# Kernel tuning notes

Measured on AMD Instinct MI355X. Metric: run time of the kernel, lower is better.

The kernel has to match this reference:

```python
import jax, jax.numpy as jnp
import numpy as np

N = 200_000   # nodes
E = 6_400_000 # edges (avg degree 32)
G = 1024      # graphs in the batch
H = 8         # hidden dim


def setup_inputs() -> dict:
    key = jax.random.key(0)
    ks = jax.random.split(key, 13)
    x = jax.random.normal(ks[0], (N, 1), dtype=jnp.float32)
    edge_index = jax.random.randint(ks[1], (2, E), 0, N, dtype=jnp.int32)
    batch = jnp.sort(jax.random.randint(ks[2], (N,), 0, G, dtype=jnp.int32))
    s = 0.3
    params = dict(
        W1a=s * jax.random.normal(ks[3], (1, H), jnp.float32),
        b1a=jnp.zeros((H,), jnp.float32),
        W1b=s * jax.random.normal(ks[4], (H, H), jnp.float32),
        b1b=jnp.zeros((H,), jnp.float32),
        W2a=s * jax.random.normal(ks[5], (H, H), jnp.float32),
        b2a=jnp.zeros((H,), jnp.float32),
        W2b=s * jax.random.normal(ks[6], (H, H), jnp.float32),
        b2b=jnp.zeros((H,), jnp.float32),
        Wfc=s * jax.random.normal(ks[7], (H, 1), jnp.float32),
        bfc=jnp.zeros((1,), jnp.float32),
    )
    return dict(x=x, edge_index=edge_index, batch=batch, **params)


def _gin_layer(h, src, dst, Wa, ba, Wb, bb):
    # GINConv with eps=0: mlp(x_i + sum_{j->i} x_j); messages aggregated at dst=edge_index[1]
    agg = jax.ops.segment_sum(h[src], dst, num_segments=N)  # [N, d]
    z = h + agg
    z = jax.nn.relu(z @ Wa + ba)
    return z @ Wb + bb


def reference(x, edge_index, batch, W1a, b1a, W1b, b1b, W2a, b2a, W2b, b2b, Wfc, bfc):
    src, dst = edge_index[0], edge_index[1]
    h = _gin_layer(x, src, dst, W1a, b1a, W1b, b1b)   # [N, 8]
    h = jax.nn.elu(h)
    h = _gin_layer(h, src, dst, W2a, b2a, W2b, b2b)   # [N, 8]
    # global mean pool over graphs
    sums = jax.ops.segment_sum(h, batch, num_segments=G)                  # [G, 8]
    counts = jax.ops.segment_sum(jnp.ones((N,), h.dtype), batch, num_segments=G)
    pooled = sums / jnp.maximum(counts, 1.0)[:, None]
    out = jax.nn.sigmoid(pooled @ Wfc + bfc)          # [G, 1]
    return out.reshape(-1)
```

## Files before the change

### kernel.cpp

```cpp
#include <hip/hip_runtime.h>
#include <hip/hip_fp8.h>
#include <math.h>

#define H 8
#define NBLKA 256
#define BTH 1024
#define BSH 8
#define BCAP 9216
#define TS 1024
#define SCAP 25600
#define POOLG 128

__device__ __forceinline__ unsigned f2fp8(float f) {
    __hip_fp8_e4m3 q(f);
    return (unsigned)q.__x;
}
__device__ __forceinline__ float fp8f(unsigned v) {
    __hip_fp8_e4m3 q;
    q.__x = (__hip_fp8_storage_t)v;
    return (float)q;
}
#if defined(__has_builtin)
#if __has_builtin(__builtin_amdgcn_cvt_pk_f32_fp8)
#define HAVE_CVT_PK_FP8 1
#endif
#endif
typedef float v2f __attribute__((ext_vector_type(2)));
__device__ __forceinline__ void unpack8(float* f, uint2 v) {
#ifdef HAVE_CVT_PK_FP8
    v2f f01 = __builtin_amdgcn_cvt_pk_f32_fp8((int)v.x, false);
    v2f f23 = __builtin_amdgcn_cvt_pk_f32_fp8((int)v.x, true);
    v2f f45 = __builtin_amdgcn_cvt_pk_f32_fp8((int)v.y, false);
    v2f f67 = __builtin_amdgcn_cvt_pk_f32_fp8((int)v.y, true);
    f[0] = f01.x; f[1] = f01.y; f[2] = f23.x; f[3] = f23.y;
    f[4] = f45.x; f[5] = f45.y; f[6] = f67.x; f[7] = f67.y;
#else
    f[0] = fp8f(v.x & 255u);         f[1] = fp8f((v.x >> 8) & 255u);
    f[2] = fp8f((v.x >> 16) & 255u); f[3] = fp8f(v.x >> 24);
    f[4] = fp8f(v.y & 255u);         f[5] = fp8f((v.y >> 8) & 255u);
    f[6] = fp8f((v.y >> 16) & 255u); f[7] = fp8f(v.y >> 24);
#endif
}
__device__ __forceinline__ void acc8(float* a, uint2 v) {
    float f[8];
    unpack8(f, v);
#pragma unroll
    for (int j = 0; j < 8; j++) a[j] += f[j];
}

__global__ __launch_bounds__(BTH) void scatterK(const int* __restrict__ ei, int E, int NB,
                                                int chunk, int* __restrict__ cursor,
                                                unsigned* __restrict__ packed) {
    __shared__ unsigned ss[SCAP];
    __shared__ int cnt[1024], sc[1024], base[1024], cur[1024];
    int t = threadIdx.x, blk = blockIdx.x;
    cnt[t] = 0;
    __syncthreads();
    int s = blk * chunk, e = min(E, s + chunk);
    for (int i = s + t; i < e; i += BTH)
        atomicAdd(&cnt[__builtin_nontemporal_load(ei + E + i) >> BSH], 1);
    __syncthreads();
    int c = cnt[t];
    sc[t] = c;
    __syncthreads();
    for (int off = 1; off < 1024; off <<= 1) {
        int v = (t >= off) ? sc[t - off] : 0;
        __syncthreads();
        sc[t] += v;
        __syncthreads();
    }
    cur[t] = sc[t] - c;
    base[t] = (t < NB && c > 0) ? atomicAdd(&cursor[t], c) : 0;
    __syncthreads();
    for (int i = s + t; i < e; i += BTH) {
        int src = __builtin_nontemporal_load(ei + i);
        int dst = __builtin_nontemporal_load(ei + E + i);
        int pos = atomicAdd(&cur[dst >> BSH], 1);
        ss[pos] = ((unsigned)src << 8) | (unsigned)(dst & 255);
    }
    __syncthreads();
    int wave = t >> 6, lane = t & 63;
    for (int j = wave; j < NB; j += (BTH >> 6)) {
        int n = cnt[j];
        int ls = sc[j] - n;
        int bs = base[j];
        int m = min(n, BCAP - bs);
        int gs = j * BCAP + bs;
        for (int k = lane; k < m; k += 64)
            packed[gs + k] = ss[ls + k];
    }
}

__global__ void sortL1K(unsigned* __restrict__ packed, const int* __restrict__ bucketCnt,
                        const float* __restrict__ x, int N,
                        const float* __restrict__ W1a, const float* __restrict__ b1a,
                        const float* __restrict__ W1b, const float* __restrict__ b1b,
                        int* __restrict__ nodeStart, uint2* __restrict__ h1) {
    __shared__ unsigned ss[BCAP];
    __shared__ float sv[BCAP];
    __shared__ int cnt[256], sb[256], cur[256];
    __shared__ float sW1a[H], sb1a[H], sW1b[H * H], sb1b[H];
    int t = threadIdx.x, b = blockIdx.x;
    if (t < 256) cnt[t] = 0;
    else if (t < 256 + H) { int j = t - 256; sW1a[j] = W1a[j]; sb1a[j] = b1a[j]; sb1b[j] = b1b[j]; }
    else if (t < 256 + H + H * H) { int j = t - 256 - H; sW1b[j] = W1b[j]; }
    __syncthreads();
    int s = b * BCAP;
    int n_e = min(bucketCnt[b], BCAP);
    unsigned pk[9];
    float xr[9];
#pragma unroll
    for (int k = 0; k < 9; k++) {
        int i = t + (k << 10);
        if (i < n_e) {
            unsigned p = packed[s + i];
            pk[k] = p;
            xr[k] = x[p >> 8];
            atomicAdd(&cnt[p & 255u], 1);
        }
    }
    __syncthreads();
    if (t < 256) sb[t] = cnt[t];
    __syncthreads();
    for (int off = 1; off < 256; off <<= 1) {
        int add = (t < 256 && t >= off) ? sb[t - off] : 0;
        __syncthreads();
        if (t < 256) sb[t] += add;
        __syncthreads();
    }
    if (t < 256) {
        int excl = sb[t] - cnt[t];
        cur[t] = excl;
        nodeStart[(b << BSH) + t] = s + excl;
    }
    __syncthreads();
#pragma unroll
    for (int k = 0; k < 9; k++) {
        int i = t + (k << 10);
        if (i < n_e) {
            unsigned p = pk[k];
            int pos = atomicAdd(&cur[p & 255u], 1);
            ss[pos] = p >> 8;
            sv[pos] = xr[k];
        }
    }
    __syncthreads();
    for (int i = t; i < n_e; i += TS) packed[s + i] = ss[i];
    int node = t >> 2, q4 = t & 3;
    int gn = (b << BSH) + node;
    float xself = x[min(gn, N - 1)];
    int lo = sb[node] - cnt[node], hi = sb[node];
    float sum = 0.f;
    for (int k = lo + q4; k < hi; k += 4) sum += sv[k];
    sum += __shfl_xor(sum, 1, 64);
    sum += __shfl_xor(sum, 2, 64);
    if (q4 == 0 && gn < N) {
        float z = xself + sum;
        float tv[H];
#pragma unroll
        for (int k = 0; k < H; k++) tv[k] = fmaxf(fmaf(z, sW1a[k], sb1a[k]), 0.f);
        float hv[H];
#pragma unroll
        for (int j = 0; j < H; j++) {
            float a = sb1b[j];
#pragma unroll
            for (int k = 0; k < H; k++) a += tv[k] * sW1b[k * H + j];
            hv[j] = a > 0.f ? a : (expf(a) - 1.f);
        }
        uint2 o;
        o.x = f2fp8(hv[0]) | (f2fp8(hv[1]) << 8) | (f2fp8(hv[2]) << 16) | (f2fp8(hv[3]) << 24);
        o.y = f2fp8(hv[4]) | (f2fp8(hv[5]) << 8) | (f2fp8(hv[6]) << 16) | (f2fp8(hv[7]) << 24);
        h1[gn] = o;
    }
}

__global__ __launch_bounds__(1024, 8) void layer2K(
        const unsigned* __restrict__ packed, const int* __restrict__ nodeStart,
        const int* __restrict__ bucketCnt, const uint2* __restrict__ h1, int N,
        const float* __restrict__ W2a, const float* __restrict__ b2a,
        const float* __restrict__ W2b, const float* __restrict__ b2b,
        const int* __restrict__ batch, float* __restrict__ sumsCnt) {
    __shared__ unsigned ss[BCAP];
    __shared__ int sNS[257];
    __shared__ float pool[POOLG * 9];
    __shared__ float sW2a[H * H], sb2a[H], sW2b[H * H], sb2b[H];
    int t = threadIdx.x, b = blockIdx.x;
    int s = b * BCAP;
    int n_e = min(bucketCnt[b], BCAP);
    for (int i = t; i < n_e; i += 1024)
        ss[i] = __builtin_nontemporal_load(packed + s + i);
    if (t < 256) sNS[t] = nodeStart[(b << BSH) + t] - s;
    if (t == 256) sNS[256] = 0;
    if (t < H) { sb2a[t] = b2a[t]; sb2b[t] = b2b[t]; }
    else if (t >= 64 && t < 64 + H * H) sW2a[t - 64] = W2a[t - 64];
    else if (t >= 192 && t < 192 + H * H) sW2b[t - 192] = W2b[t - 192];
    __syncthreads();
    if (t == 0) sNS[256] = n_e;
    __syncthreads();
    int node = t >> 2, q4 = t & 3;
    int gn = (b << BSH) + node;
    uint2 vself = h1[gn];
    int lo = sNS[node], hi = sNS[node + 1];
    float a[H] = {0.f, 0.f, 0.f, 0.f, 0.f, 0.f, 0.f, 0.f};
    for (int k0 = lo + q4; k0 < hi; k0 += 32) {
        unsigned i0 = ss[k0];
        unsigned i1 = ss[min(k0 + 4,  hi - 1)];
        unsigned i2 = ss[min(k0 + 8,  hi - 1)];
        unsigned i3 = ss[min(k0 + 12, hi - 1)];
        unsigned i4 = ss[min(k0 + 16, hi - 1)];
        unsigned i5 = ss[min(k0 + 20, hi - 1)];
        unsigned i6 = ss[min(k0 + 24, hi - 1)];
        unsigned i7 = ss[min(k0 + 28, hi - 1)];
        uint2 v0 = h1[i0];
        uint2 v1 = h1[i1];
        uint2 v2 = h1[i2];
        uint2 v3 = h1[i3];
        uint2 v4 = h1[i4];
        uint2 v5 = h1[i5];
        uint2 v6 = h1[i6];
        uint2 v7 = h1[i7];
        acc8(a, v0);
        if (k0 + 4  < hi) acc8(a, v1);
        if (k0 + 8  < hi) acc8(a, v2);
        if (k0 + 12 < hi) acc8(a, v3);
        if (k0 + 16 < hi) acc8(a, v4);
        if (k0 + 20 < hi) acc8(a, v5);
        if (k0 + 24 < hi) acc8(a, v6);
        if (k0 + 28 < hi) acc8(a, v7);
    }
#pragma unroll
    for (int j = 0; j < H; j++) {
        a[j] += __shfl_xor(a[j], 1, 64);
        a[j] += __shfl_xor(a[j], 2, 64);
    }
    bool valid = (q4 == 0) && (gn < N);
    float h2[H];
    int g = 0;
    if (valid) {
        float zs[H];
        unpack8(zs, vself);
        float z[H];
#pragma unroll
        for (int j = 0; j < H; j++) z[j] = zs[j] + a[j];
        float tv[H];
#pragma unroll
        for (int k = 0; k < H; k++) {
            float acc = sb2a[k];
#pragma unroll
            for (int j = 0; j < H; j++) acc += z[j] * sW2a[j * H + k];
            tv[k] = fmaxf(acc, 0.f);
        }
#pragma unroll
        for (int j = 0; j < H; j++) {
            float acc = sb2b[j];
#pragma unroll
            for (int k = 0; k < H; k++) acc += tv[k] * sW2b[k * H + j];
            h2[j] = acc;
        }
        g = batch[gn];
    }
    int gfirst = batch[min(b << BSH, N - 1)];
    int glast  = batch[min((b << BSH) + 255, N - 1)];
    int span = glast - gfirst + 1;
    if (span <= POOLG) {
        int span9 = span * 9;
        for (int j = t; j < span9; j += 1024) pool[j] = 0.f;
        __syncthreads();
        if (valid) {
            float* p = &pool[(g - gfirst) * 9];
#pragma unroll
            for (int j = 0; j < H; j++) atomicAdd(p + j, h2[j]);
            atomicAdd(p + 8, 1.f);
        }
        __syncthreads();
        for (int j = t; j < span9; j += 1024)
            atomicAdd(&sumsCnt[(size_t)gfirst * 9 + j], pool[j]);
    } else if (valid) {
        float* p = &sumsCnt[(size_t)g * 9];
#pragma unroll
        for (int j = 0; j < H; j++) atomicAdd(p + j, h2[j]);
        atomicAdd(p + 8, 1.f);
    }
}

__global__ void finalK(const float* __restrict__ sumsCnt, const float* __restrict__ Wfc,
                       const float* __restrict__ bfc, float* __restrict__ out, int G) {
    int g = blockIdx.x * blockDim.x + threadIdx.x;
    if (g >= G) return;
    const float* s = &sumsCnt[(size_t)g * 9];
    float c = fmaxf(s[8], 1.f);
    float dot = 0.f;
#pragma unroll
    for (int j = 0; j < H; j++) dot += s[j] * Wfc[j];
    float a = dot / c + bfc[0];
    out[g] = 1.f / (1.f + expf(-a));
}

__global__ void edge_agg1(const int* __restrict__ ei, const float* __restrict__ x,
                          float* __restrict__ agg1, int E) {
    int e = blockIdx.x * blockDim.x + threadIdx.x;
    if (e >= E) return;
    atomicAdd(&agg1[ei[E + e]], x[ei[e]]);
}
__global__ void node1F(const float* __restrict__ x, const float* __restrict__ agg1,
                       const float* __restrict__ W1a, const float* __restrict__ b1a,
                       const float* __restrict__ W1b, const float* __restrict__ b1b,
                       float* __restrict__ h1, int N) {
    int n = blockIdx.x * blockDim.x + threadIdx.x;
    if (n >= N) return;
    float z = x[n] + agg1[n];
    float tv[H];
#pragma unroll
    for (int k = 0; k < H; k++) tv[k] = fmaxf(z * W1a[k] + b1a[k], 0.f);
#pragma unroll
    for (int j = 0; j < H; j++) {
        float acc = b1b[j];
#pragma unroll
        for (int k = 0; k < H; k++) acc += tv[k] * W1b[k * H + j];
        h1[(size_t)n * H + j] = acc > 0.f ? acc : (expf(acc) - 1.f);
    }
}
__global__ void edge_agg2(const int* __restrict__ ei, const float* __restrict__ h1,
                          float* __restrict__ agg2, int E) {
    long long i = (long long)blockIdx.x * blockDim.x + threadIdx.x;
    if (i >= (long long)E * H) return;
    int e = (int)(i >> 3), k = (int)(i & 7);
    atomicAdd(&agg2[(size_t)ei[E + e] * H + k], h1[(size_t)ei[e] * H + k]);
}
__global__ void node2F(const float* __restrict__ h1, const float* __restrict__ agg2,
                       const float* __restrict__ W2a, const float* __restrict__ b2a,
                       const float* __restrict__ W2b, const float* __restrict__ b2b,
                       const int* __restrict__ batch,
                       float* __restrict__ sums, float* __restrict__ counts, int N) {
    int n = blockIdx.x * blockDim.x + threadIdx.x;
    if (n >= N) return;
    float z[H], tv[H];
#pragma unroll
    for (int j = 0; j < H; j++) z[j] = h1[(size_t)n * H + j] + agg2[(size_t)n * H + j];
#pragma unroll
    for (int k = 0; k < H; k++) {
        float a = b2a[k];
#pragma unroll
        for (int j = 0; j < H; j++) a += z[j] * W2a[j * H + k];
        tv[k] = fmaxf(a, 0.f);
    }
    int g = batch[n];
#pragma unroll
    for (int j = 0; j < H; j++) {
        float a = b2b[j];
#pragma unroll
        for (int k = 0; k < H; k++) a += tv[k] * W2b[k * H + j];
        atomicAdd(&sums[(size_t)g * H + j], a);
    }
    atomicAdd(&counts[g], 1.f);
}
__global__ void finalF(const float* __restrict__ sums, const float* __restrict__ counts,
                       const float* __restrict__ Wfc, const float* __restrict__ bfc,
                       float* __restrict__ out, int G) {
    int g = blockIdx.x * blockDim.x + threadIdx.x;
    if (g >= G) return;
    float c = fmaxf(counts[g], 1.f);
    float acc = bfc[0];
#pragma unroll
    for (int j = 0; j < H; j++) acc += (sums[(size_t)g * H + j] / c) * Wfc[j];
    out[g] = 1.f / (1.f + expf(-acc));
}

extern "C" void kernel_launch(void* const* d_in, const int* in_sizes, int n_in,
                              void* d_out, int out_size, void* d_ws, size_t ws_size,
                              hipStream_t stream) {
    const float* x    = (const float*)d_in[0];
    const int*   ei   = (const int*)d_in[1];
    const int*   batch= (const int*)d_in[2];
    const float* W1a  = (const float*)d_in[3];
    const float* b1a  = (const float*)d_in[4];
    const float* W1b  = (const float*)d_in[5];
    const float* b1b  = (const float*)d_in[6];
    const float* W2a  = (const float*)d_in[7];
    const float* b2a  = (const float*)d_in[8];
    const float* W2b  = (const float*)d_in[9];
    const float* b2b  = (const float*)d_in[10];
    const float* Wfc  = (const float*)d_in[11];
    const float* bfc  = (const float*)d_in[12];

    const int N = in_sizes[0];
    const int E = in_sizes[1] / 2;
    const int G = out_size;
    const int NB = (N + 255) >> BSH;
    const int chunk = (E + NBLKA - 1) / NBLKA;
    const int B = 256;

    auto rnd4 = [](size_t v) { return (v + 3) & ~(size_t)3; };
    size_t o_cur  = 0;
    size_t o_sc   = 1024;
    size_t zelems = o_sc + (size_t)9 * G;
    size_t o_ns   = rnd4(zelems);
    size_t o_h1   = rnd4(o_ns + ((size_t)NB << BSH) + 1);
    size_t o_pk   = rnd4(o_h1 + ((size_t)NB << BSH) * 2);
    size_t total  = o_pk + (size_t)NB * BCAP;

    bool srcFits = (N <= (1 << 18));
    bool chunkFits = (chunk <= SCAP);
    bool capOK = ((size_t)E / NB) * 10 <= (size_t)BCAP * 9;
    if (NB <= 1024 && srcFits && chunkFits && capOK && ws_size >= total * 4) {
        int*      wsi = (int*)d_ws;
        float*    wsf = (float*)d_ws;
        unsigned* wsu = (unsigned*)d_ws;
        int*      cursor    = wsi + o_cur;
        float*    sumsCnt   = wsf + o_sc;
        int*      nodeStart = wsi + o_ns;
        uint2*    h1        = (uint2*)(wsu + o_h1);
        unsigned* packed    = wsu + o_pk;

        hipMemsetAsync(d_ws, 0, zelems * 4, stream);
        scatterK<<<NBLKA, BTH, 0, stream>>>(ei, E, NB, chunk, cursor, packed);
        sortL1K<<<NB, TS, 0, stream>>>(packed, cursor, x, N, W1a, b1a, W1b, b1b,
                                       nodeStart, h1);
        layer2K<<<NB, 1024, 0, stream>>>(packed, nodeStart, cursor, h1, N,
                                         W2a, b2a, W2b, b2b, batch, sumsCnt);
        finalK<<<(G + B - 1) / B, B, 0, stream>>>(sumsCnt, Wfc, bfc, (float*)d_out, G);
    } else {
        float* ws     = (float*)d_ws;
        float* agg1   = ws;
        float* agg2   = agg1 + (size_t)N;
        float* sums   = agg2 + (size_t)8 * N;
        float* counts = sums + (size_t)8 * G;
        float* h1     = counts + (size_t)G;
        hipMemsetAsync(ws, 0, ((size_t)9 * N + (size_t)9 * G) * sizeof(float), stream);
        edge_agg1<<<(E + B - 1) / B, B, 0, stream>>>(ei, x, agg1, E);
        node1F<<<(N + B - 1) / B, B, 0, stream>>>(x, agg1, W1a, b1a, W1b, b1b, h1, N);
        long long tot = (long long)E * H;
        edge_agg2<<<(int)((tot + B - 1) / B), B, 0, stream>>>(ei, h1, agg2, E);
        node2F<<<(N + B - 1) / B, B, 0, stream>>>(h1, agg2, W2a, b2a, W2b, b2b, batch,
                                                  sums, counts, N);
        finalF<<<(G + B - 1) / B, B, 0, stream>>>(sums, counts, Wfc, bfc, (float*)d_out, G);
    }
}
```

Baseline: 254.9 us.

## Sort edges by source slice and stream h1 slices through LDS in layer 2

sortL1K now orders each destination node's edges by source slice (src>>13), using a 8192-entry count table and a 1024-wide scan. layer2K handles four buckets per block with one thread per node. It loops over source slices, staging 8192 h1 rows into LDS and consuming the matching edges from each node's sorted list. This replaces random global/L2 gathers of h1 with LDS reads. In exchange, every block re-reads all of h1, syncs once per slice, and walks its edge list serially with dependent global loads. Only about a quarter as many blocks are launched.

```diff
diff --git a/kernel.cpp b/kernel.cpp
--- a/kernel.cpp
+++ b/kernel.cpp
@@ -10,6 +10,8 @@
 #define TS 1024
 #define SCAP 25600
 #define POOLG 128
+#define KB 4
+#define SLN 8192
 
 __device__ __forceinline__ unsigned f2fp8(float f) {
     __hip_fp8_e4m3 q(f);
@@ -41,12 +43,6 @@
     f[6] = fp8f((v.y >> 16) & 255u); f[7] = fp8f(v.y >> 24);
 #endif
 }
-__device__ __forceinline__ void acc8(float* a, uint2 v) {
-    float f[8];
-    unpack8(f, v);
-#pragma unroll
-    for (int j = 0; j < 8; j++) a[j] += f[j];
-}
 
 __global__ __launch_bounds__(BTH) void scatterK(const int* __restrict__ ei, int E, int NB,
                                                 int chunk, int* __restrict__ cursor,
@@ -98,12 +94,14 @@
                         int* __restrict__ nodeStart, uint2* __restrict__ h1) {
     __shared__ unsigned ss[BCAP];
     __shared__ float sv[BCAP];
-    __shared__ int cnt[256], sb[256], cur[256];
+    __shared__ unsigned cnt[SLN];
+    __shared__ int bsum[1024];
+    __shared__ int nlo[256], nhi[256];
     __shared__ float sW1a[H], sb1a[H], sW1b[H * H], sb1b[H];
     int t = threadIdx.x, b = blockIdx.x;
-    if (t < 256) cnt[t] = 0;
-    else if (t < 256 + H) { int j = t - 256; sW1a[j] = W1a[j]; sb1a[j] = b1a[j]; sb1b[j] = b1b[j]; }
-    else if (t < 256 + H + H * H) { int j = t - 256 - H; sW1b[j] = W1b[j]; }
+    for (int i = t; i < SLN; i += TS) cnt[i] = 0;
+    if (t < H) { sW1a[t] = W1a[t]; sb1a[t] = b1a[t]; sb1b[t] = b1b[t]; }
+    else if (t >= 64 && t < 64 + H * H) sW1b[t - 64] = W1b[t - 64];
     __syncthreads();
     int s = b * BCAP;
     int n_e = min(bucketCnt[b], BCAP);
@@ -116,22 +114,29 @@
             unsigned p = packed[s + i];
             pk[k] = p;
             xr[k] = x[p >> 8];
-            atomicAdd(&cnt[p & 255u], 1);
-        }
-    }
-    __syncthreads();
-    if (t < 256) sb[t] = cnt[t];
-    __syncthreads();
-    for (int off = 1; off < 256; off <<= 1) {
-        int add = (t < 256 && t >= off) ? sb[t - off] : 0;
-        __syncthreads();
-        if (t < 256) sb[t] += add;
-        __syncthreads();
-    }
+            atomicAdd(&cnt[((p & 255u) << 5) | (p >> 21)], 1u);
+        }
+    }
+    __syncthreads();
+    unsigned r[8], s8 = 0;
+#pragma unroll
+    for (int j = 0; j < 8; j++) { r[j] = cnt[(t << 3) + j]; s8 += r[j]; }
+    bsum[t] = (int)s8;
+    __syncthreads();
+    for (int off = 1; off < 1024; off <<= 1) {
+        int v = (t >= off) ? bsum[t - off] : 0;
+        __syncthreads();
+        bsum[t] += v;
+        __syncthreads();
+    }
+    unsigned run = (unsigned)bsum[t] - s8;
+#pragma unroll
+    for (int j = 0; j < 8; j++) { cnt[(t << 3) + j] = run; run += r[j]; }
+    __syncthreads();
     if (t < 256) {
-        int excl = sb[t] - cnt[t];
-        cur[t] = excl;
-        nodeStart[(b << BSH) + t] = s + excl;
+        nlo[t] = (int)cnt[t << 5];
+        nhi[t] = (t == 255) ? n_e : (int)cnt[(t + 1) << 5];
+        nodeStart[(b << BSH) + t] = s + (int)cnt[t << 5];
     }
     __syncthreads();
 #pragma unroll
@@ -139,7 +144,7 @@
         int i = t + (k << 10);
         if (i < n_e) {
             unsigned p = pk[k];
-            int pos = atomicAdd(&cur[p & 255u], 1);
+            unsigned pos = atomicAdd(&cnt[((p & 255u) << 5) | (p >> 21)], 1u);
             ss[pos] = p >> 8;
             sv[pos] = xr[k];
         }
@@ -149,7 +154,7 @@
     int node = t >> 2, q4 = t & 3;
     int gn = (b << BSH) + node;
     float xself = x[min(gn, N - 1)];
-    int lo = sb[node] - cnt[node], hi = sb[node];
+    int lo = nlo[node], hi = nhi[node];
     float sum = 0.f;
     for (int k = lo + q4; k < hi; k += 4) sum += sv[k];
     sum += __shfl_xor(sum, 1, 64);
@@ -174,71 +179,59 @@
     }
 }
 
-__global__ __launch_bounds__(1024, 8) void layer2K(
+__global__ __launch_bounds__(1024) void layer2K(
         const unsigned* __restrict__ packed, const int* __restrict__ nodeStart,
-        const int* __restrict__ bucketCnt, const uint2* __restrict__ h1, int N,
+        const int* __restrict__ bucketCnt, const uint2* __restrict__ h1,
+        int N, int NB,
         const float* __restrict__ W2a, const float* __restrict__ b2a,
         const float* __restrict__ W2b, const float* __restrict__ b2b,
         const int* __restrict__ batch, float* __restrict__ sumsCnt) {
-    __shared__ unsigned ss[BCAP];
-    __shared__ int sNS[257];
+    __shared__ uint4 sh1q[SLN / 2];
     __shared__ float pool[POOLG * 9];
     __shared__ float sW2a[H * H], sb2a[H], sW2b[H * H], sb2b[H];
-    int t = threadIdx.x, b = blockIdx.x;
-    int s = b * BCAP;
-    int n_e = min(bucketCnt[b], BCAP);
-    for (int i = t; i < n_e; i += 1024)
-        ss[i] = __builtin_nontemporal_load(packed + s + i);
-    if (t < 256) sNS[t] = nodeStart[(b << BSH) + t] - s;
-    if (t == 256) sNS[256] = 0;
+    uint2* sh1 = (uint2*)sh1q;
+    int t = threadIdx.x, blk = blockIdx.x;
+    int bb = blk * KB + (t >> 8);
+    int node = t & 255;
+    int gn = (bb << 8) + node;
+    bool haveB = (bb < NB);
+    int sB = bb * BCAP;
+    int n_e = haveB ? min(bucketCnt[bb], BCAP) : 0;
+    int lo = haveB ? nodeStart[gn] : 0;
+    int hi = haveB ? ((node == 255) ? (sB + n_e) : nodeStart[gn + 1]) : 0;
     if (t < H) { sb2a[t] = b2a[t]; sb2b[t] = b2b[t]; }
     else if (t >= 64 && t < 64 + H * H) sW2a[t - 64] = W2a[t - 64];
     else if (t >= 192 && t < 192 + H * H) sW2b[t - 192] = W2b[t - 192];
-    __syncthreads();
-    if (t == 0) sNS[256] = n_e;
-    __syncthreads();
-    int node = t >> 2, q4 = t & 3;
-    int gn = (b << BSH) + node;
-    uint2 vself = h1[gn];
-    int lo = sNS[node], hi = sNS[node + 1];
+    int NB256 = NB << 8;
+    int NSL = (N + SLN - 1) / SLN;
     float a[H] = {0.f, 0.f, 0.f, 0.f, 0.f, 0.f, 0.f, 0.f};
-    for (int k0 = lo + q4; k0 < hi; k0 += 32) {
-        unsigned i0 = ss[k0];
-        unsigned i1 = ss[min(k0 + 4,  hi - 1)];
-        unsigned i2 = ss[min(k0 + 8,  hi - 1)];
-        unsigned i3 = ss[min(k0 + 12, hi - 1)];
-        unsigned i4 = ss[min(k0 + 16, hi - 1)];
-        unsigned i5 = ss[min(k0 + 20, hi - 1)];
-        unsigned i6 = ss[min(k0 + 24, hi - 1)];
-        unsigned i7 = ss[min(k0 + 28, hi - 1)];
-        uint2 v0 = h1[i0];
-        uint2 v1 = h1[i1];
-        uint2 v2 = h1[i2];
-        uint2 v3 = h1[i3];
-        uint2 v4 = h1[i4];
-        uint2 v5 = h1[i5];
-        uint2 v6 = h1[i6];
-        uint2 v7 = h1[i7];
-        acc8(a, v0);
-        if (k0 + 4  < hi) acc8(a, v1);
-        if (k0 + 8  < hi) acc8(a, v2);
-        if (k0 + 12 < hi) acc8(a, v3);
-        if (k0 + 16 < hi) acc8(a, v4);
-        if (k0 + 20 < hi) acc8(a, v5);
-        if (k0 + 24 < hi) acc8(a, v6);
-        if (k0 + 28 < hi) acc8(a, v7);
-    }
-#pragma unroll
-    for (int j = 0; j < H; j++) {
-        a[j] += __shfl_xor(a[j], 1, 64);
-        a[j] += __shfl_xor(a[j], 2, 64);
-    }
-    bool valid = (q4 == 0) && (gn < N);
+    int cur = lo;
+    unsigned pv = (cur < hi) ? packed[cur] : 0xFFFFFFFFu;
+    const uint4* h4 = (const uint4*)h1;
+    for (int sl = 0; sl < NSL; sl++) {
+        int g0 = sl << 13;
+        for (int i = t; i < (SLN >> 1); i += 1024) {
+            if ((g0 + (i << 1)) < NB256) sh1q[i] = h4[(g0 >> 1) + i];
+        }
+        __syncthreads();
+        while ((pv >> 13) == (unsigned)sl) {
+            uint2 v = sh1[pv & (SLN - 1u)];
+            float f[8];
+            unpack8(f, v);
+#pragma unroll
+            for (int j = 0; j < 8; j++) a[j] += f[j];
+            cur++;
+            pv = (cur < hi) ? packed[cur] : 0xFFFFFFFFu;
+        }
+        __syncthreads();
+    }
+    bool valid = haveB && (gn < N);
     float h2[H];
     int g = 0;
     if (valid) {
+        uint2 vs = h1[gn];
         float zs[H];
-        unpack8(zs, vself);
+        unpack8(zs, vs);
         float z[H];
 #pragma unroll
         for (int j = 0; j < H; j++) z[j] = zs[j] + a[j];
@@ -259,8 +252,9 @@
         }
         g = batch[gn];
     }
-    int gfirst = batch[min(b << BSH, N - 1)];
-    int glast  = batch[min((b << BSH) + 255, N - 1)];
+    int base = blk * (KB << 8);
+    int gfirst = batch[min(base, N - 1)];
+    int glast  = batch[min(base + (KB << 8) - 1, N - 1)];
     int span = glast - gfirst + 1;
     if (span <= POOLG) {
         int span9 = span * 9;
@@ -416,8 +410,9 @@
         scatterK<<<NBLKA, BTH, 0, stream>>>(ei, E, NB, chunk, cursor, packed);
         sortL1K<<<NB, TS, 0, stream>>>(packed, cursor, x, N, W1a, b1a, W1b, b1b,
                                        nodeStart, h1);
-        layer2K<<<NB, 1024, 0, stream>>>(packed, nodeStart, cursor, h1, N,
-                                         W2a, b2a, W2b, b2b, batch, sumsCnt);
+        int NBL = (NB + KB - 1) / KB;
+        layer2K<<<NBL, 1024, 0, stream>>>(packed, nodeStart, cursor, h1, N, NB,
+                                          W2a, b2a, W2b, b2b, batch, sumsCnt);
         finalK<<<(G + B - 1) / B, B, 0, stream>>>(sumsCnt, Wfc, bfc, (float*)d_out, G);
     } else {
         float* ws     = (float*)d_ws;
```

Result: slower. 309.0 us (+21.2%).
